# Optimization experiments

Hardware: AMD Instinct MI355X
Metric: run time of the kernel (lower is better)

## Reference

```python
import jax, jax.numpy as jnp
import numpy as np

B, T, D = 8, 2048, 1024

def _xavier(key, shape):
    fan_in, fan_out = shape[1], shape[0]
    limit = float(np.sqrt(6.0 / (fan_in + fan_out)))
    return jax.random.uniform(key, shape, jnp.float32, -limit, limit)

def setup_inputs() -> dict:
    key = jax.random.key(0)
    ks = jax.random.split(key, 6)
    x = jax.random.normal(ks[0], (B, T, D), jnp.float32)
    return {
        "x": x,
        "h0": jnp.zeros((B, D), jnp.float32),
        "W_in": _xavier(ks[1], (D, D)),      # in_proj.weight [d_inner, dim]
        "W_alpha": _xavier(ks[2], (D, D)),
        "d_alpha": jnp.full((D,), 0.1, jnp.float32),
        "b_alpha": jnp.full((D,), 2.0, jnp.float32),
        "W_x": _xavier(ks[3], (D, D)),
        "b_v": jnp.zeros((D,), jnp.float32),
        "W_out": _xavier(ks[4], (D, D)),     # out_proj.weight [dim, d_inner]
    }

def _silu(u):
    return u * jax.nn.sigmoid(u)

def reference(x, h0, W_in, W_alpha, d_alpha, b_alpha, W_x, b_v, W_out):
    # in_proj + SiLU: [B,T,D]
    x_proj = _silu(jnp.einsum('btd,ed->bte', x, W_in))
    # to [T,B,D] for the scan
    x_rnn = jnp.transpose(x_proj, (1, 0, 2))
    # precompute per-step gate/value GEMM contributions (as in torch ref)
    alpha_x = jnp.einsum('tbd,ed->tbe', x_rnn, W_alpha)          # [T,B,D]
    v_all = jnp.tanh(jnp.einsum('tbd,ed->tbe', x_rnn, W_x) + b_v)  # [T,B,D]

    def step(h_prev, inputs):
        ax_t, v_t = inputs
        alpha = jax.nn.sigmoid(ax_t + d_alpha * h_prev + b_alpha)
        h_new = alpha * h_prev + (1.0 - alpha) * v_t
        out_t = h_new * _silu(h_new)
        return h_new, out_t

    h_final, cell_out = jax.lax.scan(step, h0, (alpha_x, v_all))  # cell_out: [T,B,D]
    cell_out = jnp.transpose(cell_out, (1, 0, 2))                 # [B,T,D]
    output = jnp.einsum('btd,ed->bte', cell_out, W_out)
    return output, h_final
```

## Files before the change

kernel.cpp:

```cpp
#include <hip/hip_runtime.h>
#include <hip/hip_bf16.h>

typedef __attribute__((ext_vector_type(8))) short short8;
typedef __attribute__((ext_vector_type(4))) short short4v;
typedef __attribute__((ext_vector_type(4))) float f32x4;

#define Dk 1024
#define TT 2048
#define BB 8
#define MROWS (BB * TT)
#define LOG2E 1.44269504088896f

#if defined(__has_builtin)
#if __has_builtin(__builtin_amdgcn_rcpf)
#define FAST_RCP(x) __builtin_amdgcn_rcpf(x)
#endif
#if __has_builtin(__builtin_amdgcn_exp2f)
#define FAST_EXP2(x) __builtin_amdgcn_exp2f(x)
#endif
#endif
#ifndef FAST_RCP
#define FAST_RCP(x) (1.f / (x))
#endif
#ifndef FAST_EXP2
#define FAST_EXP2(x) exp2f(x)
#endif

__device__ __forceinline__ void gload_lds16(const void* g, void* l) {
    __builtin_amdgcn_global_load_lds(
        (const __attribute__((address_space(1))) void*)g,
        (__attribute__((address_space(3))) void*)l, 16, 0, 0);
}

__device__ __forceinline__ float sigmoidf_fast(float x) {
    return FAST_RCP(1.f + FAST_EXP2(-x * LOG2E));
}

__device__ __forceinline__ unsigned short bf16_bits(float x) {
    union { __hip_bfloat16 h; unsigned short u; } c;
    c.h = __float2bfloat16(x);
    return c.u;
}

__global__ __launch_bounds__(256)
void cvt_all(const float* __restrict__ x,
             const float* __restrict__ w0, const float* __restrict__ w1,
             const float* __restrict__ w2, const float* __restrict__ w3,
             __hip_bfloat16* __restrict__ xo,
             __hip_bfloat16* __restrict__ o0, __hip_bfloat16* __restrict__ o1,
             __hip_bfloat16* __restrict__ o2, __hip_bfloat16* __restrict__ o3)
{
    const int bid = blockIdx.x;
    const float* in;
    __hip_bfloat16* out;
    int base;
    if (bid < 16384) {
        in = x; out = xo; base = bid * 1024;
    } else {
        const int wbid  = bid - 16384;
        const int which = wbid >> 10;
        in  = which == 0 ? w0 : which == 1 ? w1 : which == 2 ? w2 : w3;
        out = which == 0 ? o0 : which == 1 ? o1 : which == 2 ? o2 : o3;
        base = (wbid & 1023) * 1024;
    }
    const int i = base + threadIdx.x * 4;
    const float4 v = *(const float4*)(in + i);
    __hip_bfloat16 tmp[4];
    tmp[0] = __float2bfloat16(v.x);
    tmp[1] = __float2bfloat16(v.y);
    tmp[2] = __float2bfloat16(v.z);
    tmp[3] = __float2bfloat16(v.w);
    *(short4v*)(out + i) = *(const short4v*)tmp;
}

template<int EPI>
__global__ __launch_bounds__(512, 2)
void gemm256(const __hip_bfloat16* __restrict__ A,
             const __hip_bfloat16* __restrict__ Bw,
             const float* __restrict__ bias,
             void* __restrict__ CoutV)
{
    __shared__ __align__(16) char lds[3 * 32768];

    const int tid  = threadIdx.x;
    const int bid  = blockIdx.x;
    const int nbid = (bid & 7) * 32 + (bid >> 3);
    const int tn   = nbid & 3;
    const int tm   = nbid >> 2;
    const int lane = tid & 63;
    const int w    = tid >> 6;
    const int wm   = w >> 2;
    const int wn   = w & 3;
    const int l15  = lane & 15;
    const int lq   = lane >> 4;

    const size_t baseA = (size_t)(tm * 256) * Dk;
    const size_t baseB = (size_t)(tn * 256) * Dk;

    int offA[8], offB[4];
#pragma unroll
    for (int m = 0; m < 8; ++m) {
        const int row = wm * 128 + m * 16 + l15;
        offA[m] = (row * 4 + (lq ^ (row & 3))) * 16;
    }
#pragma unroll
    for (int n = 0; n < 4; ++n) {
        const int row = wn * 64 + n * 16 + l15;
        offB[n] = 16384 + (row * 4 + (lq ^ (row & 3))) * 16;
    }

    auto stagePh = [&](int kt, char* dst, int phase) {
#pragma unroll
        for (int j = 0; j < 2; ++j) {
            const int slot = (phase * 2 + j) * 512 + tid;
            const int s    = slot & 1023;
            const int row  = s >> 2;
            const int cb   = (s & 3) ^ (row & 3);
            const __hip_bfloat16* src =
                ((slot >> 10) ? Bw + baseB : A + baseA)
                + (size_t)row * Dk + kt * 32 + cb * 8;
            gload_lds16(src, dst + slot * 16);
        }
    };

    f32x4 acc[8][4];
#pragma unroll
    for (int m = 0; m < 8; ++m)
#pragma unroll
        for (int n = 0; n < 4; ++n)
            acc[m][n] = (f32x4){0.f, 0.f, 0.f, 0.f};

    char* b0 = lds;
    char* b1 = lds + 32768;
    char* b2 = lds + 65536;

    stagePh(0, b0, 0); stagePh(0, b0, 1);
    stagePh(1, b1, 0); stagePh(1, b1, 1);
    asm volatile("s_waitcnt vmcnt(4)" ::: "memory");
    __builtin_amdgcn_s_barrier();

    char* cbuf = b0;
    char* nbuf = b1;
    char* sbuf = b2;

    for (int t = 0; t < 32; ++t) {
        short8 af[4], af2[4], bfr[4];

#pragma unroll
        for (int n = 0; n < 4; ++n)
            bfr[n] = *(const short8*)(cbuf + offB[n]);
#pragma unroll
        for (int m = 0; m < 4; ++m)
            af[m] = *(const short8*)(cbuf + offA[m]);
        if (t < 30) stagePh(t + 2, sbuf, 0);
        __builtin_amdgcn_s_barrier();
        __builtin_amdgcn_s_setprio(1);
#pragma unroll
        for (int m = 0; m < 4; ++m)
#pragma unroll
            for (int n = 0; n < 4; ++n)
                acc[m][n] = __builtin_amdgcn_mfma_f32_16x16x32_bf16(
                    af[m], bfr[n], acc[m][n], 0, 0, 0);
        __builtin_amdgcn_s_setprio(0);
        __builtin_amdgcn_s_barrier();

#pragma unroll
        for (int m = 0; m < 4; ++m)
            af2[m] = *(const short8*)(cbuf + offA[4 + m]);
        if (t < 30) stagePh(t + 2, sbuf, 1);
        __builtin_amdgcn_s_barrier();
        __builtin_amdgcn_s_setprio(1);
#pragma unroll
        for (int m = 0; m < 4; ++m)
#pragma unroll
            for (int n = 0; n < 4; ++n)
                acc[4 + m][n] = __builtin_amdgcn_mfma_f32_16x16x32_bf16(
                    af2[m], bfr[n], acc[4 + m][n], 0, 0, 0);
        __builtin_amdgcn_s_setprio(0);

        if (t < 30) {
            asm volatile("s_waitcnt vmcnt(4)" ::: "memory");
        } else if (t == 30) {
            asm volatile("s_waitcnt vmcnt(0)" ::: "memory");
        }
        if (t < 31) __builtin_amdgcn_s_barrier();

        char* tmp = cbuf; cbuf = nbuf; nbuf = sbuf; sbuf = tmp;
    }

#pragma unroll
    for (int m = 0; m < 8; ++m) {
#pragma unroll
        for (int n = 0; n < 4; ++n) {
            const int col = tn * 256 + wn * 64 + n * 16 + l15;
            float bv_ = 0.f;
            if (EPI == 6 || EPI == 7) bv_ = bias[col];
#pragma unroll
            for (int j = 0; j < 4; ++j) {
                const int rowg = tm * 256 + wm * 128 + m * 16 + lq * 4 + j;
                const size_t idx = (size_t)rowg * Dk + col;
                const float xv = acc[m][n][j];
                if constexpr (EPI == 0) {
                    ((__hip_bfloat16*)CoutV)[idx] =
                        __float2bfloat16(xv * sigmoidf_fast(xv));
                } else if constexpr (EPI == 1) {
                    ((float*)CoutV)[idx] = xv;
                } else if constexpr (EPI == 6) {
                    const float e = FAST_EXP2(-(xv + bv_) * LOG2E);
                    ((unsigned short*)CoutV)[idx * 2] = bf16_bits(e);
                } else {
                    const float y = xv + bv_;
                    const float e = FAST_EXP2(fabsf(y) * (2.f * LOG2E));
                    float tv = 1.f - 2.f * FAST_RCP(e + 1.f);
                    tv = copysignf(tv, y);
                    ((unsigned short*)CoutV)[idx * 2 + 1] = bf16_bits(tv);
                }
            }
        }
    }
}

__global__ __launch_bounds__(64)
void scan_kernel(const unsigned int* __restrict__ EV,
                 const float* __restrict__ h0,
                 const float* __restrict__ dal,
                 __hip_bfloat16* __restrict__ hout, float* __restrict__ hfin)
{
    constexpr int CH  = 32;
    constexpr int NCH = TT / CH;
    __shared__ __align__(16) unsigned int lEV[2][CH * 64];

    const int tid = threadIdx.x;
    const int bx  = blockIdx.x;
    const int b   = bx >> 4;
    const int d0  = (bx & 15) * 64;
    const int d   = d0 + tid;
    const int g   = b * Dk + d;

    float nl2 = -dal[d] * LOG2E;
    if (fabsf(nl2) < 1e-18f) nl2 = -1e-18f;
    const float inv_nl2 = 1.f / nl2;
    float ht = h0[g] * nl2;

    const size_t sbase = (size_t)b * TT * Dk + d0;

    const int sl = tid >> 4;
    const int co = (tid & 15) * 4;

    auto issue = [&](int ck, int buf) {
#pragma unroll
        for (int grp = 0; grp < 8; ++grp) {
            const size_t off = sbase + (size_t)(ck * CH + grp * 4 + sl) * Dk + co;
            gload_lds16(EV + off, (void*)&lEV[buf][grp * 256]);
        }
    };

    issue(0, 0);
    asm volatile("s_waitcnt vmcnt(0)" ::: "memory");
    __builtin_amdgcn_sched_barrier(0);

    for (int k = 0; k < NCH; ++k) {
        const int buf = k & 1;
        if (k + 1 < NCH) issue(k + 1, buf ^ 1);
        __builtin_amdgcn_sched_barrier(0);

        const size_t cbase = sbase + (size_t)(k * CH) * Dk + tid;
#pragma unroll
        for (int s = 0; s < CH; ++s) {
            const unsigned int wv = lEV[buf][s * 64 + tid];
            const float E  = __uint_as_float(wv << 16);
            const float Vt = __uint_as_float(wv & 0xffff0000u) * nl2;
            const float u  = FAST_EXP2(ht);
            const float al = FAST_RCP(fmaf(E, u, 1.f));
            ht = fmaf(al, ht - Vt, Vt);
            hout[cbase + (size_t)s * Dk] = __float2bfloat16(ht * inv_nl2);
        }
        __builtin_amdgcn_sched_barrier(0);
        if (k + 1 < NCH) {
            asm volatile("s_waitcnt vmcnt(32)" ::: "memory");
        }
        __builtin_amdgcn_sched_barrier(0);
    }

    hfin[g] = ht * inv_nl2;
}

__global__ __launch_bounds__(256)
void gpass(const __hip_bfloat16* __restrict__ hin,
           __hip_bfloat16* __restrict__ cell, int n)
{
    const int stride = gridDim.x * 256 * 8;
    for (int i = (blockIdx.x * 256 + threadIdx.x) * 8; i < n; i += stride) {
        const short8 v = *(const short8*)(hin + i);
        short8 r;
#pragma unroll
        for (int j = 0; j < 8; ++j) {
            const float x = __uint_as_float(((unsigned int)(unsigned short)v[j]) << 16);
            const float s = sigmoidf_fast(x);
            r[j] = (short)bf16_bits(x * x * s);
        }
        *(short8*)(cell + i) = r;
    }
}

extern "C" void kernel_launch(void* const* d_in, const int* in_sizes, int n_in,
                              void* d_out, int out_size, void* d_ws, size_t ws_size,
                              hipStream_t stream)
{
    const float* x     = (const float*)d_in[0];
    const float* h0    = (const float*)d_in[1];
    const float* W_in  = (const float*)d_in[2];
    const float* W_al  = (const float*)d_in[3];
    const float* d_al  = (const float*)d_in[4];
    const float* b_al  = (const float*)d_in[5];
    const float* W_x   = (const float*)d_in[6];
    const float* b_v   = (const float*)d_in[7];
    const float* W_out = (const float*)d_in[8];

    float* out  = (float*)d_out;
    float* hfin = out + (size_t)MROWS * Dk;

    char* ws = (char*)d_ws;
    const size_t bfBuf = (size_t)MROWS * Dk * sizeof(__hip_bfloat16);
    const size_t wBuf  = (size_t)Dk * Dk * sizeof(__hip_bfloat16);

    __hip_bfloat16* xb    = (__hip_bfloat16*)(ws);
    __hip_bfloat16* Winb  = (__hip_bfloat16*)(ws + bfBuf);
    __hip_bfloat16* Walb  = (__hip_bfloat16*)(ws + bfBuf + wBuf);
    __hip_bfloat16* Wxb   = (__hip_bfloat16*)(ws + bfBuf + 2 * wBuf);
    __hip_bfloat16* Woutb = (__hip_bfloat16*)(ws + bfBuf + 3 * wBuf);
    char* rest = ws + bfBuf + 4 * wBuf;
    __hip_bfloat16* xproj = (__hip_bfloat16*)rest;
    unsigned int*   EVb   = (unsigned int*)(rest + bfBuf);

    __hip_bfloat16* hbuf  = xb;
    __hip_bfloat16* cellb = xproj;

    dim3 blk(256);
    cvt_all<<<dim3(16384 + 4096), blk, 0, stream>>>(
        x, W_in, W_al, W_x, W_out, xb, Winb, Walb, Wxb, Woutb);

    dim3 ggrid(256), gblk(512);
    gemm256<0><<<ggrid, gblk, 0, stream>>>(xb,    Winb,  nullptr, xproj);
    gemm256<6><<<ggrid, gblk, 0, stream>>>(xproj, Walb,  b_al,    EVb);
    gemm256<7><<<ggrid, gblk, 0, stream>>>(xproj, Wxb,   b_v,     EVb);
    scan_kernel<<<dim3(128), dim3(64), 0, stream>>>(EVb, h0, d_al, hbuf, hfin);
    gpass<<<dim3(2048), blk, 0, stream>>>(hbuf, cellb, MROWS * Dk);
    gemm256<1><<<ggrid, gblk, 0, stream>>>(cellb, Woutb, nullptr, out);
}
```

Baseline: 279.7 us.

## Fuse gated output pass into scan kernel with a consumer wave

Removes the separate gpass kernel by adding a second wave to each scan block. Wave 0 runs the recurrence and writes fp32 h into a double-buffered LDS array. Wave 1 reads it after a per-chunk barrier, applies h*silu(h) and stores the bf16 cell output. This drops a full global round trip of the hidden-state tensor and one kernel launch, and takes the global stores off the serial scan wave. In exchange the scan wave now does a full vmcnt/lgkmcnt wait and a block barrier every chunk, which could stall the latency-bound recurrence.

```diff
diff --git a/kernel.cpp b/kernel.cpp
--- a/kernel.cpp
+++ b/kernel.cpp
@@ -220,86 +220,84 @@
     }
 }
 
-__global__ __launch_bounds__(64)
+__global__ __launch_bounds__(128)
 void scan_kernel(const unsigned int* __restrict__ EV,
                  const float* __restrict__ h0,
                  const float* __restrict__ dal,
-                 __hip_bfloat16* __restrict__ hout, float* __restrict__ hfin)
+                 __hip_bfloat16* __restrict__ cell, float* __restrict__ hfin)
 {
     constexpr int CH  = 32;
     constexpr int NCH = TT / CH;
     __shared__ __align__(16) unsigned int lEV[2][CH * 64];
-
-    const int tid = threadIdx.x;
-    const int bx  = blockIdx.x;
-    const int b   = bx >> 4;
-    const int d0  = (bx & 15) * 64;
-    const int d   = d0 + tid;
-    const int g   = b * Dk + d;
+    __shared__ __align__(16) float        lH [2][CH * 64];
+
+    const int tid  = threadIdx.x;
+    const int wave = tid >> 6;
+    const int lane = tid & 63;
+    const int bx   = blockIdx.x;
+    const int b    = bx >> 4;
+    const int d0   = (bx & 15) * 64;
+    const int d    = d0 + lane;
+    const int g    = b * Dk + d;
 
     float nl2 = -dal[d] * LOG2E;
     if (fabsf(nl2) < 1e-18f) nl2 = -1e-18f;
     const float inv_nl2 = 1.f / nl2;
-    float ht = h0[g] * nl2;
 
     const size_t sbase = (size_t)b * TT * Dk + d0;
 
-    const int sl = tid >> 4;
-    const int co = (tid & 15) * 4;
-
-    auto issue = [&](int ck, int buf) {
-#pragma unroll
-        for (int grp = 0; grp < 8; ++grp) {
-            const size_t off = sbase + (size_t)(ck * CH + grp * 4 + sl) * Dk + co;
-            gload_lds16(EV + off, (void*)&lEV[buf][grp * 256]);
-        }
-    };
-
-    issue(0, 0);
-    asm volatile("s_waitcnt vmcnt(0)" ::: "memory");
-    __builtin_amdgcn_sched_barrier(0);
-
-    for (int k = 0; k < NCH; ++k) {
-        const int buf = k & 1;
-        if (k + 1 < NCH) issue(k + 1, buf ^ 1);
+    if (wave == 0) {
+        float ht = h0[g] * nl2;
+
+        const int sl = lane >> 4;
+        const int co = (lane & 15) * 4;
+        auto issue = [&](int ck, int buf) {
+#pragma unroll
+            for (int grp = 0; grp < 8; ++grp) {
+                const size_t off = sbase + (size_t)(ck * CH + grp * 4 + sl) * Dk + co;
+                gload_lds16(EV + off, (void*)&lEV[buf][grp * 256]);
+            }
+        };
+
+        issue(0, 0);
+        asm volatile("s_waitcnt vmcnt(0)" ::: "memory");
         __builtin_amdgcn_sched_barrier(0);
 
-        const size_t cbase = sbase + (size_t)(k * CH) * Dk + tid;
-#pragma unroll
-        for (int s = 0; s < CH; ++s) {
-            const unsigned int wv = lEV[buf][s * 64 + tid];
-            const float E  = __uint_as_float(wv << 16);
-            const float Vt = __uint_as_float(wv & 0xffff0000u) * nl2;
-            const float u  = FAST_EXP2(ht);
-            const float al = FAST_RCP(fmaf(E, u, 1.f));
-            ht = fmaf(al, ht - Vt, Vt);
-            hout[cbase + (size_t)s * Dk] = __float2bfloat16(ht * inv_nl2);
-        }
-        __builtin_amdgcn_sched_barrier(0);
-        if (k + 1 < NCH) {
-            asm volatile("s_waitcnt vmcnt(32)" ::: "memory");
-        }
-        __builtin_amdgcn_sched_barrier(0);
-    }
-
-    hfin[g] = ht * inv_nl2;
-}
-
-__global__ __launch_bounds__(256)
-void gpass(const __hip_bfloat16* __restrict__ hin,
-           __hip_bfloat16* __restrict__ cell, int n)
-{
-    const int stride = gridDim.x * 256 * 8;
-    for (int i = (blockIdx.x * 256 + threadIdx.x) * 8; i < n; i += stride) {
-        const short8 v = *(const short8*)(hin + i);
-        short8 r;
-#pragma unroll
-        for (int j = 0; j < 8; ++j) {
-            const float x = __uint_as_float(((unsigned int)(unsigned short)v[j]) << 16);
-            const float s = sigmoidf_fast(x);
-            r[j] = (short)bf16_bits(x * x * s);
-        }
-        *(short8*)(cell + i) = r;
+        for (int k = 0; k < NCH; ++k) {
+            const int buf = k & 1;
+            if (k + 1 < NCH) issue(k + 1, buf ^ 1);
+            __builtin_amdgcn_sched_barrier(0);
+
+#pragma unroll
+            for (int s = 0; s < CH; ++s) {
+                const unsigned int wv = lEV[buf][s * 64 + lane];
+                const float E  = __uint_as_float(wv << 16);
+                const float Vt = __uint_as_float(wv & 0xffff0000u) * nl2;
+                const float u  = FAST_EXP2(ht);
+                const float al = FAST_RCP(fmaf(E, u, 1.f));
+                ht = fmaf(al, ht - Vt, Vt);
+                lH[buf][s * 64 + lane] = ht;
+            }
+            __builtin_amdgcn_sched_barrier(0);
+            asm volatile("s_waitcnt vmcnt(0) lgkmcnt(0)" ::: "memory");
+            __builtin_amdgcn_sched_barrier(0);
+            __builtin_amdgcn_s_barrier();
+        }
+        hfin[g] = ht * inv_nl2;
+    } else {
+        for (int k = 0; k < NCH; ++k) {
+            __builtin_amdgcn_s_barrier();
+            __builtin_amdgcn_sched_barrier(0);
+            const int buf = k & 1;
+            const size_t cbase = sbase + (size_t)(k * CH) * Dk + lane;
+#pragma unroll
+            for (int s = 0; s < CH; ++s) {
+                const float ht = lH[buf][s * 64 + lane];
+                const float h  = ht * inv_nl2;
+                const float sg = FAST_RCP(1.f + FAST_EXP2(-h * LOG2E));
+                cell[cbase + (size_t)s * Dk] = __float2bfloat16(h * h * sg);
+            }
+        }
     }
 }
 
@@ -333,7 +331,6 @@
     __hip_bfloat16* xproj = (__hip_bfloat16*)rest;
     unsigned int*   EVb   = (unsigned int*)(rest + bfBuf);
 
-    __hip_bfloat16* hbuf  = xb;
     __hip_bfloat16* cellb = xproj;
 
     dim3 blk(256);
@@ -344,7 +341,6 @@
     gemm256<0><<<ggrid, gblk, 0, stream>>>(xb,    Winb,  nullptr, xproj);
     gemm256<6><<<ggrid, gblk, 0, stream>>>(xproj, Walb,  b_al,    EVb);
     gemm256<7><<<ggrid, gblk, 0, stream>>>(xproj, Wxb,   b_v,     EVb);
-    scan_kernel<<<dim3(128), dim3(64), 0, stream>>>(EVb, h0, d_al, hbuf, hfin);
-    gpass<<<dim3(2048), blk, 0, stream>>>(hbuf, cellb, MROWS * Dk);
+    scan_kernel<<<dim3(128), dim3(128), 0, stream>>>(EVb, h0, d_al, cellb, hfin);
     gemm256<1><<<ggrid, gblk, 0, stream>>>(cellb, Woutb, nullptr, out);
 }
```

After: 276.7 us. No clear change (-1.0%).
